# Optimization experiments

Hardware: AMD Instinct MI355X
Metric: run time of the kernel (lower is better)

## Reference

```python
import jax, jax.numpy as jnp
import numpy as np

N_QUBITS = 10      # = hidden_dim; state vector has 2**10 = 1024 amplitudes
T, B, D = 128, 256, 64
H = N_QUBITS
DIM = 2 ** N_QUBITS


def _rx(theta):
    # RX(t) = [[cos(t/2), -i sin(t/2)], [-i sin(t/2), cos(t/2)]]; theta scalar or (B,)
    c = jnp.cos(theta / 2).astype(jnp.complex64)
    s = (-1j) * jnp.sin(theta / 2).astype(jnp.complex64)
    return jnp.stack([jnp.stack([c, s], -1), jnp.stack([s, c], -1)], -2)


def _ry(theta):
    c = jnp.cos(theta / 2)
    s = jnp.sin(theta / 2)
    return jnp.stack([jnp.stack([c, -s], -1), jnp.stack([s, c], -1)], -2).astype(jnp.complex64)


def _rz(theta):
    em = jnp.exp(-0.5j * theta.astype(jnp.complex64))
    ep = jnp.exp(0.5j * theta.astype(jnp.complex64))
    z = jnp.zeros_like(em)
    return jnp.stack([jnp.stack([em, z], -1), jnp.stack([z, ep], -1)], -2)


def _apply_1q(state, mat, w):
    # state: (B, 2^n) complex; wire 0 is the most-significant axis (torchquantum layout)
    b = state.shape[0]
    s = state.reshape(b, 2 ** w, 2, -1)
    if mat.ndim == 2:
        out = jnp.einsum('ij,bljr->blir', mat, s)
    else:  # batched encoding angles: mat (B,2,2)
        out = jnp.einsum('bij,bljr->blir', mat, s)
    return out.reshape(b, -1)


def _apply_cnot(state, a, bq):
    # control a < target bq: flip target axis in the control=1 block
    b = state.shape[0]
    s = state.reshape(b, 2 ** a, 2, 2 ** (bq - a - 1), 2, -1)
    new = jnp.stack([s[:, :, 0], s[:, :, 1, :, ::-1]], axis=2)
    return new.reshape(b, -1)


def qgate(x, params):
    # x: (B, n) classical features -> PauliZ expectations per wire (B, n)
    n = N_QUBITS
    b = x.shape[0]
    state = jnp.zeros((b, 2 ** n), jnp.complex64).at[:, 0].set(1.0 + 0.0j)
    for w in range(n):                       # RX encoding of input features
        state = _apply_1q(state, _rx(x[:, w]), w)
    for w in range(n):                       # parameterized RX, RY, RZ per wire
        state = _apply_1q(state, _rx(params[w, 0]), w)
        state = _apply_1q(state, _ry(params[w, 1]), w)
        state = _apply_1q(state, _rz(params[w, 2]), w)
    for a in range(n - 1):                   # CNOT chain entanglement
        state = _apply_cnot(state, a, a + 1)
    probs = jnp.real(state * jnp.conj(state))
    zs = []
    for w in range(n):                       # <Z_w> = P(bit_w=0) - P(bit_w=1)
        p = probs.reshape(b, 2 ** w, 2, -1)
        zs.append(p[:, :, 0, :].sum((1, 2)) - p[:, :, 1, :].sum((1, 2)))
    return jnp.stack(zs, axis=1)


def setup_inputs() -> dict:
    key = jax.random.key(0)
    ks = jax.random.split(key, 16)
    scale = 1.0 / np.sqrt(D + H)
    inp = {'inputs': jax.random.normal(ks[0], (T, B, D), jnp.float32)}
    for i, g in enumerate(['f', 'i', 'u', 'o']):
        inp['W' + g] = jax.random.normal(ks[1 + 3 * i], (H, D + H), jnp.float32) * scale
        inp['b' + g] = jax.random.normal(ks[2 + 3 * i], (H,), jnp.float32) * scale
        inp['p' + g] = jax.random.normal(ks[3 + 3 * i], (H, 3), jnp.float32)
    inp['ln_g'] = jnp.ones((H,), jnp.float32)
    inp['ln_b'] = jnp.zeros((H,), jnp.float32)
    return inp


def reference(inputs, Wf, bf, pf, Wi, bi, pi, Wu, bu, pu, Wo, bo, po, ln_g, ln_b):
    b = inputs.shape[1]

    def step(carry, x):
        hx, cx = carry
        comb = jnp.concatenate([x, hx], axis=1)
        f = jax.nn.sigmoid(qgate(comb @ Wf.T + bf, pf))
        i = jax.nn.sigmoid(qgate(comb @ Wi.T + bi, pi))
        g = jnp.tanh(qgate(comb @ Wu.T + bu, pu))
        o = jax.nn.sigmoid(qgate(comb @ Wo.T + bo, po))
        cx2 = f * cx + i * g
        h = o * jnp.tanh(cx2) + hx  # residual skip
        mu = h.mean(-1, keepdims=True)
        var = ((h - mu) ** 2).mean(-1, keepdims=True)
        h = (h - mu) / jnp.sqrt(var + 1e-5) * ln_g + ln_b  # LayerNorm
        # dropout: identity in eval mode
        return (h, cx2), h

    init = (jnp.zeros((b, H), jnp.float32), jnp.zeros((b, H), jnp.float32))
    (hx, cx), ys = jax.lax.scan(step, init, inputs)
    return ys, hx, cx
```

## Files before the change

### kernel.cpp

```cpp
#include <hip/hip_runtime.h>
#include <math.h>


#define T_STEPS 128
#define B_SZ    256
#define D_IN    64
#define H_SZ    10
#define COMB    74
#define ZPAD    132

template<int CTRL>
__device__ __forceinline__ float dpp_mov(float old_, float src) {
    return __int_as_float(__builtin_amdgcn_update_dpp(
        __float_as_int(old_), __float_as_int(src), CTRL, 0xF, 0xF, false));
}
#define DPP_ROW_SHR(n) (0x110 + (n))
#define DPP_ROW_ROR(n) (0x120 + (n))

__device__ __forceinline__ float rdlane(float v, int lane) {
    return __int_as_float(__builtin_amdgcn_readlane(__float_as_int(v), lane));
}
__device__ __forceinline__ float frcp(float x) { return __builtin_amdgcn_rcpf(x); }

__device__ __forceinline__ float tanh_pade(float x) {
    float x2  = x * x;
    float num = x * fmaf(x2, (x2 + 105.f), 945.f);
    float den = fmaf(x2, fmaf(x2, 15.f, 420.f), 945.f);
    return num * frcp(den);
}

__global__ __launch_bounds__(128) void qlstm_fused(
    const float* __restrict__ x,
    const float* __restrict__ Wf, const float* __restrict__ bf, const float* __restrict__ pf,
    const float* __restrict__ Wi, const float* __restrict__ bi, const float* __restrict__ pi,
    const float* __restrict__ Wu, const float* __restrict__ bu, const float* __restrict__ pu,
    const float* __restrict__ Wo, const float* __restrict__ bo, const float* __restrict__ po,
    const float* __restrict__ ln_g, const float* __restrict__ ln_b,
    float* __restrict__ ys, float* __restrict__ outH, float* __restrict__ outC)
{
    __shared__ __align__(16) float Wl[40 * 64];
    __shared__ __align__(16) float Zl[40 * ZPAD];
    __shared__ __align__(16) float ys_l[T_STEPS * H_SZ + 64];
    __shared__ float bl[40];

    const int tid = threadIdx.x;
    const int b   = blockIdx.x;

    float xr[64];
    const float4* xin = (const float4*)(x + ((size_t)tid * B_SZ + b) * D_IN);
#pragma unroll
    for (int k = 0; k < 16; k++) {
        float4 v = xin[k];
        xr[4*k+0] = v.x; xr[4*k+1] = v.y; xr[4*k+2] = v.z; xr[4*k+3] = v.w;
    }

#pragma unroll
    for (int k = 0; k < 20; k++) {
        int idx = k * 128 + tid;
        int r   = idx >> 6;
        int col = idx & 63;
        const float* Wp; int w;
        if      (r < 10) { Wp = Wf; w = r;      }
        else if (r < 20) { Wp = Wi; w = r - 10; }
        else if (r < 30) { Wp = Wu; w = r - 20; }
        else             { Wp = Wo; w = r - 30; }
        Wl[idx] = Wp[w * COMB + col];
    }
    if (tid < 40) {
        int r = tid;
        const float* bp; int w;
        if      (r < 10) { bp = bf; w = r;      }
        else if (r < 20) { bp = bi; w = r - 10; }
        else if (r < 30) { bp = bu; w = r - 20; }
        else             { bp = bo; w = r - 30; }
        bl[tid] = bp[w];
    }
    __syncthreads();

#pragma unroll
    for (int gw = 0; gw < 40; gw++) {
        float a = bl[gw];
        const float4* wr4 = (const float4*)(Wl + gw * 64);
#pragma unroll
        for (int d4 = 0; d4 < 16; d4++) {
            float4 wv = wr4[d4];
            a = fmaf(xr[4*d4+0], wv.x, a);
            a = fmaf(xr[4*d4+1], wv.y, a);
            a = fmaf(xr[4*d4+2], wv.z, a);
            a = fmaf(xr[4*d4+3], wv.w, a);
        }
        Zl[gw * ZPAD + tid] = a;
    }
    __syncthreads();

    if (tid >= 64) return;

    const int lane = tid;
    const int g    = lane >> 4;
    const int w    = lane & 15;
    const bool act = (w < H_SZ);

    const float* Ws[4] = {Wf, Wi, Wu, Wo};
    const float* ps[4] = {pf, pi, pu, po};

    float whp[H_SZ];
    float S = 0.f, A = 0.f;
#pragma unroll
    for (int j = 0; j < H_SZ; j++) {
        float whj = act ? Ws[g][w * COMB + D_IN + j] : 0.f;
        whp[j] = whj * ln_g[j];
        S += whp[j];
        A  = fmaf(whj, ln_b[j], A);
    }
    const float p0  = act ? ps[g][w * 3 + 0] : 0.f;
    const float cp1 = act ? __cosf(ps[g][w * 3 + 1]) : 1.f;
    const float lng = act ? ln_g[w] : 0.f;
    const float lnb = act ? ln_b[w] : 0.f;
    const float s0 = (g == 2) ? 0.f : 0.5f;
    const float s1 = (g == 2) ? 1.f : 0.5f;
    const float sc = (g == 2) ? 1.f : 0.5f;

    float hn = 0.f;
    float cc = 0.f;
    float hterm = 0.f;

    const int gwl = g * 10 + (act ? w : 9);
    const float* zb = Zl + (size_t)gwl * ZPAD;
    float4 zb0 = *(const float4*)(zb);
    float4 zb1 = *(const float4*)(zb + 4);

    float* ysl = ys_l + lane;

    for (int gq = 0; gq < T_STEPS / 4; gq++) {
        float4 zc = zb0;
        zb0 = zb1;
        const int nl = (gq + 2 < T_STEPS / 4) ? gq + 2 : T_STEPS / 4 - 1;
        zb1 = *(const float4*)(zb + (size_t)nl * 4);

        float zs[4] = {zc.x, zc.y, zc.z, zc.w};
#pragma unroll
        for (int j = 0; j < 4; j++) {
            const int t = gq * 4 + j;
            float z = zs[j] + hterm;

            float prod = cp1 * __cosf(p0 + z);
            asm("s_nop 1\n\t"
                "v_mul_f32_dpp %0, %0, %0 row_shr:1 row_mask:0xf bank_mask:0xf\n\t"
                "s_nop 1\n\t"
                "v_mul_f32_dpp %0, %0, %0 row_shr:2 row_mask:0xf bank_mask:0xf\n\t"
                "s_nop 1\n\t"
                "v_mul_f32_dpp %0, %0, %0 row_shr:4 row_mask:0xf bank_mask:0xf\n\t"
                "s_nop 1\n\t"
                "v_mul_f32_dpp %0, %0, %0 row_shr:8 row_mask:0xf bank_mask:0xf"
                : "+v"(prod));

            float av = fmaf(s1, tanh_pade(sc * prod), s0);

            float a_ = av, b_ = av;
            asm("s_nop 1\n\t"
                "v_permlane32_swap_b32 %0, %1" : "+v"(a_), "+v"(b_));
            float F_ = a_, I_ = a_;
            asm("s_nop 1\n\t"
                "v_permlane16_swap_b32 %0, %1" : "+v"(F_), "+v"(I_));
            float U_ = b_, O_ = b_;
            asm("s_nop 1\n\t"
                "v_permlane16_swap_b32 %0, %1" : "+v"(U_), "+v"(O_));

            cc = fmaf(F_, cc, I_ * U_);
            float tc   = tanh_pade(cc);
            float hraw = fmaf(O_, tc, hn);

            float v1 = act ? hraw : 0.f;
            float v2 = v1 * v1;
            asm("s_nop 1\n\t"
                "v_add_f32_dpp %0, %0, %0 row_ror:8 row_mask:0xf bank_mask:0xf\n\t"
                "v_add_f32_dpp %1, %1, %1 row_ror:8 row_mask:0xf bank_mask:0xf\n\t"
                "s_nop 0\n\t"
                "v_add_f32_dpp %0, %0, %0 row_ror:4 row_mask:0xf bank_mask:0xf\n\t"
                "v_add_f32_dpp %1, %1, %1 row_ror:4 row_mask:0xf bank_mask:0xf\n\t"
                "s_nop 0\n\t"
                "v_add_f32_dpp %0, %0, %0 row_ror:2 row_mask:0xf bank_mask:0xf\n\t"
                "v_add_f32_dpp %1, %1, %1 row_ror:2 row_mask:0xf bank_mask:0xf\n\t"
                "s_nop 0\n\t"
                "v_add_f32_dpp %0, %0, %0 row_ror:1 row_mask:0xf bank_mask:0xf\n\t"
                "v_add_f32_dpp %1, %1, %1 row_ror:1 row_mask:0xf bank_mask:0xf"
                : "+v"(v1), "+v"(v2));

            float d0 = whp[0] * rdlane(hraw, 0);
            float d1 = whp[1] * rdlane(hraw, 1);
            d0 = fmaf(whp[2], rdlane(hraw, 2), d0);
            d1 = fmaf(whp[3], rdlane(hraw, 3), d1);
            d0 = fmaf(whp[4], rdlane(hraw, 4), d0);
            d1 = fmaf(whp[5], rdlane(hraw, 5), d1);
            d0 = fmaf(whp[6], rdlane(hraw, 6), d0);
            d1 = fmaf(whp[7], rdlane(hraw, 7), d1);
            d0 = fmaf(whp[8], rdlane(hraw, 8), d0);
            d1 = fmaf(whp[9], rdlane(hraw, 9), d1);
            float D = d0 + d1;

            float mu   = v1 * 0.1f;
            float varr = fmaxf(fmaf(v2, 0.1f, -mu * mu), 0.f);
            float rstd = __builtin_amdgcn_rsqf(varr + 1e-5f);

            hn    = fmaf((hraw - mu) * rstd, lng, lnb);
            hterm = fmaf(rstd, fmaf(-mu, S, D), A);

            ysl[t * H_SZ] = hn;
        }
    }

#pragma unroll
    for (int k = 0; k < 20; k++) {
        int idx = k * 64 + lane;
        int t   = idx / H_SZ;
        int ww  = idx - t * H_SZ;
        ys[(size_t)t * B_SZ * H_SZ + (size_t)b * H_SZ + ww] = ys_l[idx];
    }

    if (lane < H_SZ) {
        outH[b * H_SZ + lane] = hn;
        outC[b * H_SZ + lane] = cc;
    }
}

extern "C" void kernel_launch(void* const* d_in, const int* in_sizes, int n_in,
                              void* d_out, int out_size, void* d_ws, size_t ws_size,
                              hipStream_t stream)
{
    const float* x    = (const float*)d_in[0];
    const float* Wf   = (const float*)d_in[1];
    const float* bf   = (const float*)d_in[2];
    const float* pf   = (const float*)d_in[3];
    const float* Wi   = (const float*)d_in[4];
    const float* bi   = (const float*)d_in[5];
    const float* pi   = (const float*)d_in[6];
    const float* Wu   = (const float*)d_in[7];
    const float* bu   = (const float*)d_in[8];
    const float* pu   = (const float*)d_in[9];
    const float* Wo   = (const float*)d_in[10];
    const float* bo   = (const float*)d_in[11];
    const float* po   = (const float*)d_in[12];
    const float* ln_g = (const float*)d_in[13];
    const float* ln_b = (const float*)d_in[14];

    float* ys   = (float*)d_out;
    float* outH = ys + (size_t)T_STEPS * B_SZ * H_SZ;
    float* outC = outH + (size_t)B_SZ * H_SZ;

    qlstm_fused<<<B_SZ, 128, 0, stream>>>(
        x, Wf, bf, pf, Wi, bi, pi, Wu, bu, pu, Wo, bo, po,
        ln_g, ln_b, ys, outH, outC);
}
```

Measured before the change: 126.9 us.

## Interleave two batch recurrences per wavefront to hide serial latency

Each block now handles two batch elements. A single 64-lane wave runs both LSTM recurrences interleaved step by step, so the independent dependency chains can hide each other's DPP, permlane and transcendental latency. The projection phase uses 256 threads to compute Z for both elements, the grid is halved, and LDS usage roughly doubles. The risk is that half as many blocks (128) on a GPU with many CUs leaves most CUs idle, so total time may track the longer per-wave serial chain.

```diff
diff --git a/kernel.cpp b/kernel.cpp
--- a/kernel.cpp
+++ b/kernel.cpp
@@ -8,14 +8,8 @@
 #define H_SZ    10
 #define COMB    74
 #define ZPAD    132
-
-template<int CTRL>
-__device__ __forceinline__ float dpp_mov(float old_, float src) {
-    return __int_as_float(__builtin_amdgcn_update_dpp(
-        __float_as_int(old_), __float_as_int(src), CTRL, 0xF, 0xF, false));
-}
-#define DPP_ROW_SHR(n) (0x110 + (n))
-#define DPP_ROW_ROR(n) (0x120 + (n))
+#define ZTILE   (40 * ZPAD)
+#define YSTILE  (T_STEPS * H_SZ + 64)
 
 __device__ __forceinline__ float rdlane(float v, int lane) {
     return __int_as_float(__builtin_amdgcn_readlane(__float_as_int(v), lane));
@@ -29,7 +23,80 @@
     return num * frcp(den);
 }
 
-__global__ __launch_bounds__(128) void qlstm_fused(
+__device__ __forceinline__ void qstep(
+    float zsv, int t, float& hn, float& cc, float& hterm, float* ysl,
+    float cp1, float p0, float s0, float s1, float sc,
+    const float (&whp)[H_SZ], float Sln, float Aln, float lng, float lnb,
+    bool act)
+{
+    float z = zsv + hterm;
+
+    float prod = cp1 * __cosf(p0 + z);
+    asm("s_nop 1\n\t"
+        "v_mul_f32_dpp %0, %0, %0 row_shr:1 row_mask:0xf bank_mask:0xf\n\t"
+        "s_nop 1\n\t"
+        "v_mul_f32_dpp %0, %0, %0 row_shr:2 row_mask:0xf bank_mask:0xf\n\t"
+        "s_nop 1\n\t"
+        "v_mul_f32_dpp %0, %0, %0 row_shr:4 row_mask:0xf bank_mask:0xf\n\t"
+        "s_nop 1\n\t"
+        "v_mul_f32_dpp %0, %0, %0 row_shr:8 row_mask:0xf bank_mask:0xf"
+        : "+v"(prod));
+
+    float av = fmaf(s1, tanh_pade(sc * prod), s0);
+
+    float a_ = av, b_ = av;
+    asm("s_nop 1\n\t"
+        "v_permlane32_swap_b32 %0, %1" : "+v"(a_), "+v"(b_));
+    float F_ = a_, I_ = a_;
+    asm("s_nop 1\n\t"
+        "v_permlane16_swap_b32 %0, %1" : "+v"(F_), "+v"(I_));
+    float U_ = b_, O_ = b_;
+    asm("s_nop 1\n\t"
+        "v_permlane16_swap_b32 %0, %1" : "+v"(U_), "+v"(O_));
+
+    cc = fmaf(F_, cc, I_ * U_);
+    float tc   = tanh_pade(cc);
+    float hraw = fmaf(O_, tc, hn);
+
+    float v1 = act ? hraw : 0.f;
+    float v2 = v1 * v1;
+    asm("s_nop 1\n\t"
+        "v_add_f32_dpp %0, %0, %0 row_ror:8 row_mask:0xf bank_mask:0xf\n\t"
+        "v_add_f32_dpp %1, %1, %1 row_ror:8 row_mask:0xf bank_mask:0xf\n\t"
+        "s_nop 0\n\t"
+        "v_add_f32_dpp %0, %0, %0 row_ror:4 row_mask:0xf bank_mask:0xf\n\t"
+        "v_add_f32_dpp %1, %1, %1 row_ror:4 row_mask:0xf bank_mask:0xf\n\t"
+        "s_nop 0\n\t"
+        "v_add_f32_dpp %0, %0, %0 row_ror:2 row_mask:0xf bank_mask:0xf\n\t"
+        "v_add_f32_dpp %1, %1, %1 row_ror:2 row_mask:0xf bank_mask:0xf\n\t"
+        "s_nop 0\n\t"
+        "v_add_f32_dpp %0, %0, %0 row_ror:1 row_mask:0xf bank_mask:0xf\n\t"
+        "v_add_f32_dpp %1, %1, %1 row_ror:1 row_mask:0xf bank_mask:0xf"
+        : "+v"(v1), "+v"(v2));
+
+    float d0 = whp[0] * rdlane(hraw, 0);
+    float d1 = whp[1] * rdlane(hraw, 1);
+    d0 = fmaf(whp[2], rdlane(hraw, 2), d0);
+    d1 = fmaf(whp[3], rdlane(hraw, 3), d1);
+    d0 = fmaf(whp[4], rdlane(hraw, 4), d0);
+    d1 = fmaf(whp[5], rdlane(hraw, 5), d1);
+    d0 = fmaf(whp[6], rdlane(hraw, 6), d0);
+    d1 = fmaf(whp[7], rdlane(hraw, 7), d1);
+    d0 = fmaf(whp[8], rdlane(hraw, 8), d0);
+    d1 = fmaf(whp[9], rdlane(hraw, 9), d1);
+    float D = d0 + d1;
+
+    float mu   = v1 * 0.1f;
+    float varr = fmaxf(fmaf(v2, 0.1f, -mu * mu), 0.f);
+    float rstd = __builtin_amdgcn_rsqf(varr + 1e-5f);
+
+    hn    = fmaf((hraw - mu) * rstd, lng, lnb);
+    hterm = fmaf(rstd, fmaf(-mu, Sln, D), Aln);
+
+    ysl[t * H_SZ] = hn;
+}
+
+__global__ __launch_bounds__(256) void qlstm_fused(
     const float* __restrict__ x,
     const float* __restrict__ Wf, const float* __restrict__ bf, const float* __restrict__ pf,
     const float* __restrict__ Wi, const float* __restrict__ bi, const float* __restrict__ pi,
@@ -39,15 +106,17 @@
     float* __restrict__ ys, float* __restrict__ outH, float* __restrict__ outC)
 {
     __shared__ __align__(16) float Wl[40 * 64];
-    __shared__ __align__(16) float Zl[40 * ZPAD];
-    __shared__ __align__(16) float ys_l[T_STEPS * H_SZ + 64];
+    __shared__ __align__(16) float Zl[2 * ZTILE];
+    __shared__ __align__(16) float ys_l[2 * YSTILE];
     __shared__ float bl[40];
 
     const int tid = threadIdx.x;
-    const int b   = blockIdx.x;
+    const int bs  = tid >> 7;
+    const int tt  = tid & 127;
+    const int b0  = blockIdx.x * 2;
 
     float xr[64];
-    const float4* xin = (const float4*)(x + ((size_t)tid * B_SZ + b) * D_IN);
+    const float4* xin = (const float4*)(x + ((size_t)tt * B_SZ + (b0 + bs)) * D_IN);
 #pragma unroll
     for (int k = 0; k < 16; k++) {
         float4 v = xin[k];
@@ -55,8 +124,8 @@
     }
 
 #pragma unroll
-    for (int k = 0; k < 20; k++) {
-        int idx = k * 128 + tid;
+    for (int k = 0; k < 10; k++) {
+        int idx = k * 256 + tid;
         int r   = idx >> 6;
         int col = idx & 63;
         const float* Wp; int w;
@@ -77,6 +146,7 @@
     }
     __syncthreads();
 
+    float* Zt = Zl + bs * ZTILE;
 #pragma unroll
     for (int gw = 0; gw < 40; gw++) {
         float a = bl[gw];
@@ -89,7 +159,7 @@
             a = fmaf(xr[4*d4+2], wv.z, a);
             a = fmaf(xr[4*d4+3], wv.w, a);
         }
-        Zl[gw * ZPAD + tid] = a;
+        Zt[gw * ZPAD + tt] = a;
     }
     __syncthreads();
 
@@ -120,92 +190,36 @@
     const float s1 = (g == 2) ? 1.f : 0.5f;
     const float sc = (g == 2) ? 1.f : 0.5f;
 
-    float hn = 0.f;
-    float cc = 0.f;
-    float hterm = 0.f;
+    float hn0 = 0.f, cc0 = 0.f, ht0 = 0.f;
+    float hn1 = 0.f, cc1 = 0.f, ht1 = 0.f;
 
     const int gwl = g * 10 + (act ? w : 9);
-    const float* zb = Zl + (size_t)gwl * ZPAD;
-    float4 zb0 = *(const float4*)(zb);
-    float4 zb1 = *(const float4*)(zb + 4);
-
-    float* ysl = ys_l + lane;
+    const float* zbA = Zl + gwl * ZPAD;
+    const float* zbB = Zl + ZTILE + gwl * ZPAD;
+    float4 a_zb0 = *(const float4*)(zbA);
+    float4 a_zb1 = *(const float4*)(zbA + 4);
+    float4 b_zb0 = *(const float4*)(zbB);
+    float4 b_zb1 = *(const float4*)(zbB + 4);
+
+    float* yslA = ys_l + lane;
+    float* yslB = ys_l + YSTILE + lane;
 
     for (int gq = 0; gq < T_STEPS / 4; gq++) {
-        float4 zc = zb0;
-        zb0 = zb1;
+        float4 zcA = a_zb0; a_zb0 = a_zb1;
+        float4 zcB = b_zb0; b_zb0 = b_zb1;
         const int nl = (gq + 2 < T_STEPS / 4) ? gq + 2 : T_STEPS / 4 - 1;
-        zb1 = *(const float4*)(zb + (size_t)nl * 4);
-
-        float zs[4] = {zc.x, zc.y, zc.z, zc.w};
+        a_zb1 = *(const float4*)(zbA + (size_t)nl * 4);
+        b_zb1 = *(const float4*)(zbB + (size_t)nl * 4);
+
+        float zsA[4] = {zcA.x, zcA.y, zcA.z, zcA.w};
+        float zsB[4] = {zcB.x, zcB.y, zcB.z, zcB.w};
 #pragma unroll
         for (int j = 0; j < 4; j++) {
             const int t = gq * 4 + j;
-            float z = zs[j] + hterm;
-
-            float prod = cp1 * __cosf(p0 + z);
-            asm("s_nop 1\n\t"
-                "v_mul_f32_dpp %0, %0, %0 row_shr:1 row_mask:0xf bank_mask:0xf\n\t"
-                "s_nop 1\n\t"
-                "v_mul_f32_dpp %0, %0, %0 row_shr:2 row_mask:0xf bank_mask:0xf\n\t"
-                "s_nop 1\n\t"
-                "v_mul_f32_dpp %0, %0, %0 row_shr:4 row_mask:0xf bank_mask:0xf\n\t"
-                "s_nop 1\n\t"
-                "v_mul_f32_dpp %0, %0, %0 row_shr:8 row_mask:0xf bank_mask:0xf"
-                : "+v"(prod));
-
-            float av = fmaf(s1, tanh_pade(sc * prod), s0);
-
-            float a_ = av, b_ = av;
-            asm("s_nop 1\n\t"
-                "v_permlane32_swap_b32 %0, %1" : "+v"(a_), "+v"(b_));
-            float F_ = a_, I_ = a_;
-            asm("s_nop 1\n\t"
-                "v_permlane16_swap_b32 %0, %1" : "+v"(F_), "+v"(I_));
-            float U_ = b_, O_ = b_;
-            asm("s_nop 1\n\t"
-                "v_permlane16_swap_b32 %0, %1" : "+v"(U_), "+v"(O_));
-
-            cc = fmaf(F_, cc, I_ * U_);
-            float tc   = tanh_pade(cc);
-            float hraw = fmaf(O_, tc, hn);
-
-            float v1 = act ? hraw : 0.f;
-            float v2 = v1 * v1;
-            asm("s_nop 1\n\t"
-                "v_add_f32_dpp %0, %0, %0 row_ror:8 row_mask:0xf bank_mask:0xf\n\t"
-                "v_add_f32_dpp %1, %1, %1 row_ror:8 row_mask:0xf bank_mask:0xf\n\t"
-                "s_nop 0\n\t"
-                "v_add_f32_dpp %0, %0, %0 row_ror:4 row_mask:0xf bank_mask:0xf\n\t"
-                "v_add_f32_dpp %1, %1, %1 row_ror:4 row_mask:0xf bank_mask:0xf\n\t"
-                "s_nop 0\n\t"
-                "v_add_f32_dpp %0, %0, %0 row_ror:2 row_mask:0xf bank_mask:0xf\n\t"
-                "v_add_f32_dpp %1, %1, %1 row_ror:2 row_mask:0xf bank_mask:0xf\n\t"
-                "s_nop 0\n\t"
-                "v_add_f32_dpp %0, %0, %0 row_ror:1 row_mask:0xf bank_mask:0xf\n\t"
-                "v_add_f32_dpp %1, %1, %1 row_ror:1 row_mask:0xf bank_mask:0xf"
-                : "+v"(v1), "+v"(v2));
-
-            float d0 = whp[0] * rdlane(hraw, 0);
-            float d1 = whp[1] * rdlane(hraw, 1);
-            d0 = fmaf(whp[2], rdlane(hraw, 2), d0);
-            d1 = fmaf(whp[3], rdlane(hraw, 3), d1);
-            d0 = fmaf(whp[4], rdlane(hraw, 4), d0);
-            d1 = fmaf(whp[5], rdlane(hraw, 5), d1);
-            d0 = fmaf(whp[6], rdlane(hraw, 6), d0);
-            d1 = fmaf(whp[7], rdlane(hraw, 7), d1);
-            d0 = fmaf(whp[8], rdlane(hraw, 8), d0);
-            d1 = fmaf(whp[9], rdlane(hraw, 9), d1);
-            float D = d0 + d1;
-
-            float mu   = v1 * 0.1f;
-            float varr = fmaxf(fmaf(v2, 0.1f, -mu * mu), 0.f);
-            float rstd = __builtin_amdgcn_rsqf(varr + 1e-5f);
-
-            hn    = fmaf((hraw - mu) * rstd, lng, lnb);
-            hterm = fmaf(rstd, fmaf(-mu, S, D), A);
-
-            ysl[t * H_SZ] = hn;
+            qstep(zsA[j], t, hn0, cc0, ht0, yslA,
+                  cp1, p0, s0, s1, sc, whp, S, A, lng, lnb, act);
+            qstep(zsB[j], t, hn1, cc1, ht1, yslB,
+                  cp1, p0, s0, s1, sc, whp, S, A, lng, lnb, act);
         }
     }
 
@@ -214,12 +228,16 @@
         int idx = k * 64 + lane;
         int t   = idx / H_SZ;
         int ww  = idx - t * H_SZ;
-        ys[(size_t)t * B_SZ * H_SZ + (size_t)b * H_SZ + ww] = ys_l[idx];
+        size_t go = (size_t)t * B_SZ * H_SZ + (size_t)b0 * H_SZ + ww;
+        ys[go]            = ys_l[idx];
+        ys[go + H_SZ]     = ys_l[YSTILE + idx];
     }
 
     if (lane < H_SZ) {
-        outH[b * H_SZ + lane] = hn;
-        outC[b * H_SZ + lane] = cc;
+        outH[(b0 + 0) * H_SZ + lane] = hn0;
+        outC[(b0 + 0) * H_SZ + lane] = cc0;
+        outH[(b0 + 1) * H_SZ + lane] = hn1;
+        outC[(b0 + 1) * H_SZ + lane] = cc1;
     }
 }
 
@@ -247,7 +265,7 @@
     float* outH = ys + (size_t)T_STEPS * B_SZ * H_SZ;
     float* outC = outH + (size_t)B_SZ * H_SZ;
 
-    qlstm_fused<<<B_SZ, 128, 0, stream>>>(
+    qlstm_fused<<<B_SZ / 2, 256, 0, stream>>>(
         x, Wf, bf, pf, Wi, bi, pi, Wu, bu, pu, Wo, bo, po,
         ln_g, ln_b, ys, outH, outC);
 }
```

Result: slower. 150.2 us (+18.4%).
